# Kernel tuning notes

Hardware: AMD Instinct MI355X
Metric: run time of the kernel (lower is better)

The kernel has to match this reference:

```python
import jax, jax.numpy as jnp
import numpy as np

E, H, I, R, T, TOPK = 8, 1024, 2816, 8, 4096, 2
SCALING = 2.0  # lora_alpha / r = 16 / 8


def setup_inputs() -> dict:
    key = jax.random.key(0)
    ks = jax.random.split(key, 12)
    inp = {
        "hidden_states": jax.random.normal(ks[0], (T, H), dtype=jnp.float32),
        "routing_weights": jax.random.uniform(ks[1], (T, TOPK), dtype=jnp.float32),
        "selected_experts": jax.random.randint(ks[2], (T, TOPK), 0, E),
        # frozen base expert weights, (G, K, N) layout
        "gate_proj": jax.random.normal(ks[3], (E, H, I), dtype=jnp.float32) * 0.02,
        "up_proj": jax.random.normal(ks[4], (E, H, I), dtype=jnp.float32) * 0.02,
        "down_proj": jax.random.normal(ks[5], (E, I, H), dtype=jnp.float32) * 0.02,
        # LoRA adapters, A: [E, in, r], B: [E, r, out]  (B random, not zero, so delta is exercised)
        "gate_A": jax.random.normal(ks[6], (E, H, R), dtype=jnp.float32) * 0.02,
        "gate_B": jax.random.normal(ks[7], (E, R, I), dtype=jnp.float32) * 0.02,
        "up_A": jax.random.normal(ks[8], (E, H, R), dtype=jnp.float32) * 0.02,
        "up_B": jax.random.normal(ks[9], (E, R, I), dtype=jnp.float32) * 0.02,
        "down_A": jax.random.normal(ks[10], (E, I, R), dtype=jnp.float32) * 0.02,
        "down_B": jax.random.normal(ks[11], (E, R, H), dtype=jnp.float32) * 0.02,
    }
    return inp


def _moe_lora_forward(x, routing_weights, selected_experts,
                      gate_proj, up_proj, down_proj,
                      gate_A, gate_B, up_A, up_B, down_A, down_B):
    # combine weights per (token, expert): [T, E]
    combine = jnp.sum(
        jax.nn.one_hot(selected_experts, E, dtype=x.dtype) * routing_weights[..., None],
        axis=1,
    )
    out = jnp.zeros_like(x)
    for e in range(E):  # static small loop over experts
        g = x @ gate_proj[e] + SCALING * ((x @ gate_A[e]) @ gate_B[e])
        u = x @ up_proj[e] + SCALING * ((x @ up_A[e]) @ up_B[e])
        h = jax.nn.silu(g) * u  # [T, I]
        y = h @ down_proj[e] + SCALING * ((h @ down_A[e]) @ down_B[e])  # [T, H]
        out = out + combine[:, e:e + 1] * y
    return out


def reference(hidden_states, routing_weights, selected_experts,
              gate_proj, up_proj, down_proj,
              gate_A, gate_B, up_A, up_B, down_A, down_B):
    return _moe_lora_forward(hidden_states, routing_weights, selected_experts,
                             gate_proj, up_proj, down_proj,
                             gate_A, gate_B, up_A, up_B, down_A, down_B)
```

## Files before the change

### kernel.cpp

```cpp
#include <hip/hip_runtime.h>
#include <stdint.h>

#define T_TOK 4096
#define NE 8
#define HH 1024
#define II 2816
#define HE 1056
#define IEW 2944
#define HT 23
#define RRK 8
#define NPAIR (T_TOK*2)
#define ROWCAP 10240
#define MT_MAX 40
#define SCAL 2.0f

typedef short v8s __attribute__((ext_vector_type(8)));
typedef float v4f __attribute__((ext_vector_type(4)));

__device__ __forceinline__ unsigned short f2bf(float f){
  union { float f; unsigned u; } c; c.f = f;
  unsigned u = c.u;
  u += 0x7FFFu + ((u >> 16) & 1u);
  return (unsigned short)(u >> 16);
}
__device__ __forceinline__ float bf2f(unsigned short h){
  union { unsigned u; float f; } c; c.u = ((unsigned)h) << 16;
  return c.f;
}
__device__ __forceinline__ void gload16(const void* g, void* l){
  __builtin_amdgcn_global_load_lds(
      (const __attribute__((address_space(1))) unsigned int*)g,
      (__attribute__((address_space(3))) unsigned int*)l, 16, 0, 0);
}
__device__ __forceinline__ void fence_(){ asm volatile("" ::: "memory"); }

__global__ void route_count(const int* __restrict__ sel, int* __restrict__ counts,
                            int* __restrict__ bases, int* __restrict__ tile_e,
                            int* __restrict__ tile_r0){
  __shared__ int c[NE];
  int tid = threadIdx.x;
  if (tid < NE) c[tid] = 0;
  __syncthreads();
  for (int p = tid; p < NPAIR; p += 256) atomicAdd(&c[sel[p]], 1);
  __syncthreads();
  if (tid == 0){
    int b = 0;
    for (int e = 0; e < NE; e++){ counts[e] = c[e]; bases[e] = b; b += ((c[e] + 255) >> 8) << 8; }
    bases[NE] = b;
    int t = 0;
    for (int e = 0; e < NE; e++){
      int nt = (c[e] + 255) >> 8;
      for (int i = 0; i < nt; i++){ tile_e[t] = e; tile_r0[t] = bases[e] + i * 256; t++; }
    }
    for (; t < MT_MAX; t++){ tile_e[t] = -1; tile_r0[t] = 0; }
  }
}

__global__ void route_fill(const int* __restrict__ sel, const float* __restrict__ rw,
                           const int* __restrict__ bases,
                           int* __restrict__ row_token, int* __restrict__ row_expert,
                           float* __restrict__ row_w, int* __restrict__ pair2row){
  int e = blockIdx.x;
  int lane = threadIdx.x;
  if (e == NE){
    for (int idx = bases[NE] + lane; idx < ROWCAP; idx += 64){
      row_token[idx] = -1; row_expert[idx] = 0; row_w[idx] = 0.f;
    }
    return;
  }
  int base = bases[e];
  int cnt = 0;
  for (int chunk = 0; chunk < NPAIR; chunk += 64){
    int p = chunk + lane;
    bool m = (sel[p] == e);
    unsigned long long mask = __ballot(m);
    if (m){
      int pos = __popcll(mask & ((1ull << lane) - 1ull));
      int dst = base + cnt + pos;
      row_token[dst] = p >> 1;
      row_expert[dst] = e;
      row_w[dst] = rw[p];
      pair2row[p] = dst;
    }
    cnt += __popcll(mask);
  }
  int nb = bases[e + 1];
  for (int idx = base + cnt + lane; idx < nb; idx += 64){
    row_token[idx] = -1; row_expert[idx] = e; row_w[idx] = 0.f;
  }
}

__global__ void transpose_cvt(const float* __restrict__ W, unsigned short* __restrict__ Wt,
                              int K, int N, int KE){
  int e = blockIdx.y;
  int tilesK = K >> 6;
  int kt = (blockIdx.x % tilesK) * 64;
  int nt = (blockIdx.x / tilesK) * 64;
  __shared__ float tile[64][65];
  int tid = threadIdx.x;
  int r = tid >> 2;
  int c0 = (tid & 3) * 16;
  const float* src = W + (size_t)e * K * N + (size_t)(kt + r) * N + nt + c0;
  #pragma unroll
  for (int i = 0; i < 4; i++){
    float4 v = *(const float4*)(src + i * 4);
    tile[r][c0 + i*4 + 0] = v.x; tile[r][c0 + i*4 + 1] = v.y;
    tile[r][c0 + i*4 + 2] = v.z; tile[r][c0 + i*4 + 3] = v.w;
  }
  __syncthreads();
  union { unsigned short us[16]; uint4 q[2]; } pk;
  #pragma unroll
  for (int j = 0; j < 16; j++) pk.us[j] = f2bf(tile[c0 + j][r]);
  unsigned short* dst = Wt + (size_t)e * N * KE + (size_t)(nt + r) * KE + kt + c0;
  *(uint4*)(dst) = pk.q[0];
  *(uint4*)(dst + 8) = pk.q[1];
}

__global__ void ext_fill_pair(unsigned short* __restrict__ Wtg, unsigned short* __restrict__ Wtu,
                              const float* __restrict__ gB, const float* __restrict__ uB){
  int idx = blockIdx.x * 256 + threadIdx.x;
  if (idx >= NE * II) return;
  int e = idx / II, n = idx % II;
  unsigned short* g = Wtg + ((size_t)e * II + n) * HE + HH;
  unsigned short* u = Wtu + ((size_t)e * II + n) * HE + HH;
  #pragma unroll
  for (int j = 0; j < 8; j++){
    g[j] = f2bf(gB[((size_t)e * RRK + j) * II + n]);
    u[j] = 0;
    g[8 + j] = 0;
    u[8 + j] = f2bf(uB[((size_t)e * RRK + j) * II + n]);
  }
  #pragma unroll
  for (int j = 16; j < 32; j++){ g[j] = 0; u[j] = 0; }
}

__global__ void ext_fill_down(unsigned short* __restrict__ Wtd, const float* __restrict__ dB){
  int idx = blockIdx.x * 256 + threadIdx.x;
  if (idx >= NE * HH) return;
  int e = idx / HH, n = idx % HH;
  unsigned short* d = Wtd + ((size_t)e * HH + n) * IEW + II;
  #pragma unroll
  for (int j = 0; j < 8; j++) d[j] = f2bf(dB[((size_t)e * RRK + j) * HH + n]);
  for (int j = 8; j < 128; j++) d[j] = 0;
}

__global__ void gather_x(const float* __restrict__ x, const int* __restrict__ row_token,
                         unsigned short* __restrict__ Xg){
  int p = blockIdx.x; int tid = threadIdx.x;
  int tok = row_token[p];
  float4 v = make_float4(0.f, 0.f, 0.f, 0.f);
  if (tok >= 0) v = *(const float4*)(x + (size_t)tok * HH + tid * 4);
  uint2 o;
  o.x = (unsigned)f2bf(v.x) | ((unsigned)f2bf(v.y) << 16);
  o.y = (unsigned)f2bf(v.z) | ((unsigned)f2bf(v.w) << 16);
  *(uint2*)(Xg + (size_t)p * HE + tid * 4) = o;
}

__global__ void xa_kernel(const float* __restrict__ x, const float* __restrict__ gA,
                          const float* __restrict__ uA, const int* __restrict__ row_token,
                          const int* __restrict__ row_expert,
                          unsigned short* __restrict__ Xg){
  int p = blockIdx.x; int tid = threadIdx.x;
  int tok = row_token[p]; int e = row_expert[p];
  float ag[8], au[8];
  #pragma unroll
  for (int r = 0; r < 8; r++){ ag[r] = 0.f; au[r] = 0.f; }
  if (tok >= 0){
    int k0 = tid * 4;
    float4 xv = *(const float4*)(x + (size_t)tok * HH + k0);
    const float* pg = gA + ((size_t)e * HH + k0) * RRK;
    const float* pu = uA + ((size_t)e * HH + k0) * RRK;
    float xs[4] = {xv.x, xv.y, xv.z, xv.w};
    #pragma unroll
    for (int j = 0; j < 4; j++){
      #pragma unroll
      for (int r = 0; r < 8; r++){
        ag[r] += xs[j] * pg[j * RRK + r];
        au[r] += xs[j] * pu[j * RRK + r];
      }
    }
  }
  __shared__ float redg[8][4], redu[8][4];
  int lane = tid & 63, wv = tid >> 6;
  #pragma unroll
  for (int r = 0; r < 8; r++){
    float v1 = ag[r], v2 = au[r];
    for (int off = 32; off > 0; off >>= 1){ v1 += __shfl_down(v1, off); v2 += __shfl_down(v2, off); }
    if (lane == 0){ redg[r][wv] = v1; redu[r][wv] = v2; }
  }
  __syncthreads();
  if (tid < 8)
    Xg[(size_t)p * HE + HH + tid] = f2bf(SCAL * (redg[tid][0] + redg[tid][1] + redg[tid][2] + redg[tid][3]));
  else if (tid < 16){
    int r = tid - 8;
    Xg[(size_t)p * HE + HH + 8 + r] = f2bf(SCAL * (redu[r][0] + redu[r][1] + redu[r][2] + redu[r][3]));
  } else if (tid < 32){
    Xg[(size_t)p * HE + HH + tid] = 0;
  }
}

__global__ void ha_kernel(const unsigned short* __restrict__ hbuf, const float* __restrict__ dA,
                          const int* __restrict__ row_expert, unsigned short* __restrict__ hout){
  int p = blockIdx.x; int tid = threadIdx.x;
  int e = row_expert[p];
  float a[8];
  #pragma unroll
  for (int r = 0; r < 8; r++) a[r] = 0.f;
  for (int i = 0; i < 11; i++){
    int k = i * 256 + tid;
    float hv = bf2f(hbuf[(size_t)(k >> 7) * (ROWCAP * 128) + (size_t)p * 128 + (k & 127)]);
    const float* pd = dA + ((size_t)e * II + k) * RRK;
    #pragma unroll
    for (int r = 0; r < 8; r++) a[r] += hv * pd[r];
  }
  __shared__ float red[8][4];
  int lane = tid & 63, wv = tid >> 6;
  #pragma unroll
  for (int r = 0; r < 8; r++){
    float v = a[r];
    for (int off = 32; off > 0; off >>= 1) v += __shfl_down(v, off);
    if (lane == 0) red[r][wv] = v;
  }
  __syncthreads();
  unsigned short* ext = hout + (size_t)22 * (ROWCAP * 128) + (size_t)p * 128;
  if (tid < 8)
    ext[tid] = f2bf(SCAL * (red[tid][0] + red[tid][1] + red[tid][2] + red[tid][3]));
  else if (tid < 128)
    ext[tid] = 0;
}

__launch_bounds__(512, 2)
__global__ void gemm1_kernel(const unsigned short* __restrict__ Xg,
                             const unsigned short* __restrict__ Wtg,
                             const unsigned short* __restrict__ Wtu,
                             const int* __restrict__ tile_e,
                             const int* __restrict__ tile_r0,
                             unsigned short* __restrict__ hbuf){
  int hw = blockIdx.x;
  int lg = (hw & 7) * 110 + (hw >> 3);
  int mt = lg / 22;
  int n0 = (lg % 22) * 128;

  int e = tile_e[mt];
  if (e < 0) return;
  int row0 = tile_r0[mt];

  __shared__ unsigned short lds[2][4 * 4096];
  int tid = threadIdx.x;
  int lane = tid & 63;
  int w = tid >> 6;
  int wm = w >> 1;
  int wn = w & 1;
  int g = lane >> 4, r16 = lane & 15;

  const unsigned short* srcA = Xg + (size_t)row0 * HE;
  const unsigned short* srcG = Wtg + ((size_t)e * II + n0) * HE;
  const unsigned short* srcU = Wtu + ((size_t)e * II + n0) * HE;

  v4f accg[4][4], accu[4][4];
  #pragma unroll
  for (int i = 0; i < 4; i++)
    #pragma unroll
    for (int j = 0; j < 4; j++){
      accg[i][j] = (v4f){0.f, 0.f, 0.f, 0.f};
      accu[i][j] = (v4f){0.f, 0.f, 0.f, 0.f};
    }

  int uA0 = tid, uA1 = tid + 512;
  int rA0 = uA0 >> 2, rA1 = uA1 >> 2;
  size_t gA0 = (size_t)rA0 * HE + ((uA0 & 3) ^ ((rA0 >> 1) & 3)) * 8;
  size_t gA1 = (size_t)rA1 * HE + ((uA1 & 3) ^ ((rA1 >> 1) & 3)) * 8;
  int lA0 = (uA0 & ~63) * 8, lA1 = (uA1 & ~63) * 8;
  int rB = tid >> 2;
  size_t gB = (size_t)rB * HE + ((tid & 3) ^ ((rB >> 1) & 3)) * 8;
  int lB = (tid & ~63) * 8;

  const int NT = HE / 32;

  {
    unsigned short* buf = lds[0];
    gload16(srcA + gA0, buf + lA0);
    gload16(srcA + gA1, buf + lA1);
    gload16(srcG + gB, buf + 8192 + lB);
    gload16(srcU + gB, buf + 12288 + lB);
  }

  for (int t = 0; t < NT; t++){
    if (t + 1 < NT){
      unsigned short* nbuf = lds[(t + 1) & 1];
      int ks = (t + 1) * 32;
      gload16(srcA + gA0 + ks, nbuf + lA0);
      gload16(srcA + gA1 + ks, nbuf + lA1);
      gload16(srcG + gB + ks, nbuf + 8192 + lB);
      gload16(srcU + gB + ks, nbuf + 12288 + lB);
      asm volatile("s_waitcnt vmcnt(4)" ::: "memory");
    } else {
      asm volatile("s_waitcnt vmcnt(0)" ::: "memory");
    }
    __builtin_amdgcn_s_barrier();
    fence_();
    const unsigned short* buf = lds[t & 1];
    v8s a[4], bg[4], bu[4];
    #pragma unroll
    for (int f = 0; f < 4; f++){
      int rowA = wm * 64 + f * 16 + r16;
      int ca = g ^ ((rowA >> 1) & 3);
      a[f] = *(const v8s*)(buf + rowA * 32 + ca * 8);
      int rowB = wn * 64 + f * 16 + r16;
      int cb = g ^ ((rowB >> 1) & 3);
      bg[f] = *(const v8s*)(buf + 8192 + rowB * 32 + cb * 8);
      bu[f] = *(const v8s*)(buf + 12288 + rowB * 32 + cb * 8);
    }
    #pragma unroll
    for (int fm = 0; fm < 4; fm++)
      #pragma unroll
      for (int fn = 0; fn < 4; fn++){
        accg[fm][fn] = __builtin_amdgcn_mfma_f32_16x16x32_bf16(a[fm], bg[fn], accg[fm][fn], 0, 0, 0);
        accu[fm][fn] = __builtin_amdgcn_mfma_f32_16x16x32_bf16(a[fm], bu[fn], accu[fm][fn], 0, 0, 0);
      }
    fence_();
    __builtin_amdgcn_s_barrier();
    fence_();
  }

  unsigned short* sh = (unsigned short*)lds;
  #pragma unroll
  for (int fm = 0; fm < 4; fm++)
    #pragma unroll
    for (int fn = 0; fn < 4; fn++)
      #pragma unroll
      for (int r = 0; r < 4; r++){
        int lrow = wm * 64 + fm * 16 + g * 4 + r;
        int lcol = wn * 64 + fn * 16 + r16;
        float gg = accg[fm][fn][r];
        float uu = accu[fm][fn][r];
        float hh = (gg / (1.f + __expf(-gg))) * uu;
        int ch = (lcol >> 3) ^ (lrow & 7);
        sh[lrow * 128 + ch * 8 + (lcol & 7)] = f2bf(hh);
      }
  __syncthreads();
  unsigned short* dst = hbuf + ((size_t)(n0 >> 7) * ROWCAP + row0) * 128;
  #pragma unroll
  for (int pass = 0; pass < 8; pass++){
    int idx2 = pass * 512 + tid;
    int row = idx2 >> 4;
    int ch = idx2 & 15;
    int chs = ch ^ (row & 7);
    v8s val = *(const v8s*)(sh + row * 128 + chs * 8);
    *(v8s*)(dst + row * 128 + ch * 8) = val;
  }
}

__launch_bounds__(512, 2)
__global__ void gemm2_kernel(const unsigned short* __restrict__ hbuf,
                             const unsigned short* __restrict__ Wtd,
                             const int* __restrict__ tile_e,
                             const int* __restrict__ tile_r0,
                             const float* __restrict__ row_w,
                             float* __restrict__ Y){
  int hw = blockIdx.x;
  int lg = (hw & 7) * 40 + (hw >> 3);
  int mt = lg / 8;
  int n0 = (lg % 8) * 128;

  int e = tile_e[mt];
  if (e < 0) return;
  int row0 = tile_r0[mt];

  __shared__ unsigned short lds[2][3 * 4096];
  int tid = threadIdx.x;
  int lane = tid & 63;
  int w = tid >> 6;
  int wm = w >> 1, wn = w & 1;
  int g = lane >> 4, r16 = lane & 15;

  const unsigned short* srcA = hbuf + (size_t)row0 * 128;
  const unsigned short* srcB = Wtd + ((size_t)e * HH + n0) * IEW;

  v4f acc[4][4];
  #pragma unroll
  for (int i = 0; i < 4; i++)
    #pragma unroll
    for (int j = 0; j < 4; j++) acc[i][j] = (v4f){0.f, 0.f, 0.f, 0.f};

  int uA0 = tid, uA1 = tid + 512;
  int rA0 = uA0 >> 2, rA1 = uA1 >> 2;
  int cA0 = (uA0 & 3) ^ ((rA0 >> 1) & 3), cA1 = (uA1 & 3) ^ ((rA1 >> 1) & 3);
  size_t aoff0 = (size_t)rA0 * 128 + cA0 * 8;
  size_t aoff1 = (size_t)rA1 * 128 + cA1 * 8;
  int lA0 = (uA0 & ~63) * 8, lA1 = (uA1 & ~63) * 8;
  int rB = tid >> 2;
  int cB = (tid & 3) ^ ((rB >> 1) & 3);
  size_t boff = (size_t)rB * IEW + cB * 8;
  int lB = (tid & ~63) * 8;

  const int NT = IEW / 32;

  {
    unsigned short* buf = lds[0];
    gload16(srcA + aoff0, buf + lA0);
    gload16(srcA + aoff1, buf + lA1);
    gload16(srcB + boff, buf + 8192 + lB);
  }

  for (int t = 0; t < NT; t++){
    if (t + 1 < NT){
      unsigned short* nbuf = lds[(t + 1) & 1];
      int ks = (t + 1) * 32;
      size_t abase = (size_t)(ks >> 7) * (ROWCAP * 128) + (ks & 127);
      gload16(srcA + abase + aoff0, nbuf + lA0);
      gload16(srcA + abase + aoff1, nbuf + lA1);
      gload16(srcB + (size_t)ks + boff, nbuf + 8192 + lB);
      asm volatile("s_waitcnt vmcnt(3)" ::: "memory");
    } else {
      asm volatile("s_waitcnt vmcnt(0)" ::: "memory");
    }
    __builtin_amdgcn_s_barrier();
    fence_();
    const unsigned short* buf = lds[t & 1];
    v8s a[4], b[4];
    #pragma unroll
    for (int f = 0; f < 4; f++){
      int rowA = wm * 64 + f * 16 + r16;
      int ca = g ^ ((rowA >> 1) & 3);
      a[f] = *(const v8s*)(buf + rowA * 32 + ca * 8);
      int rowB = wn * 64 + f * 16 + r16;
      int cb = g ^ ((rowB >> 1) & 3);
      b[f] = *(const v8s*)(buf + 8192 + rowB * 32 + cb * 8);
    }
    #pragma unroll
    for (int fm = 0; fm < 4; fm++)
      #pragma unroll
      for (int fn = 0; fn < 4; fn++)
        acc[fm][fn] = __builtin_amdgcn_mfma_f32_16x16x32_bf16(a[fm], b[fn], acc[fm][fn], 0, 0, 0);
    fence_();
    __builtin_amdgcn_s_barrier();
    fence_();
  }

  #pragma unroll
  for (int fm = 0; fm < 4; fm++){
    #pragma unroll
    for (int r = 0; r < 4; r++){
      int lrow = wm * 64 + fm * 16 + g * 4 + r;
      int grow = row0 + lrow;
      float wgt = row_w[grow];
      #pragma unroll
      for (int fn = 0; fn < 4; fn++){
        int lcol = wn * 64 + fn * 16 + r16;
        Y[(size_t)grow * HH + n0 + lcol] = wgt * acc[fm][fn][r];
      }
    }
  }
}

__global__ void combine_kernel(const float* __restrict__ Y, const int* __restrict__ pair2row,
                               float* __restrict__ out){
  int t = blockIdx.x;
  int c = threadIdx.x * 4;
  int r0 = pair2row[2 * t];
  int r1 = pair2row[2 * t + 1];
  float4 a = *(const float4*)(Y + (size_t)r0 * HH + c);
  float4 b = *(const float4*)(Y + (size_t)r1 * HH + c);
  float4 o = make_float4(a.x + b.x, a.y + b.y, a.z + b.z, a.w + b.w);
  *(float4*)(out + (size_t)t * HH + c) = o;
}

extern "C" void kernel_launch(void* const* d_in, const int* in_sizes, int n_in,
                              void* d_out, int out_size, void* d_ws, size_t ws_size,
                              hipStream_t stream){
  const float* x         = (const float*)d_in[0];
  const float* rw        = (const float*)d_in[1];
  const int*   sel       = (const int*)d_in[2];
  const float* gate_proj = (const float*)d_in[3];
  const float* up_proj   = (const float*)d_in[4];
  const float* down_proj = (const float*)d_in[5];
  const float* gate_A    = (const float*)d_in[6];
  const float* gate_B    = (const float*)d_in[7];
  const float* up_A      = (const float*)d_in[8];
  const float* up_B      = (const float*)d_in[9];
  const float* down_A    = (const float*)d_in[10];
  const float* down_B    = (const float*)d_in[11];
  float* out = (float*)d_out;
  char* ws = (char*)d_ws;

  constexpr size_t OFF_COUNTS = 0;
  constexpr size_t OFF_BASES  = 256;
  constexpr size_t OFF_TILE_E = 512;
  constexpr size_t OFF_TILE_R0 = 1024;
  constexpr size_t OFF_ROWTOK = 2048;
  constexpr size_t OFF_ROWEXP = OFF_ROWTOK + (size_t)ROWCAP * 4;
  constexpr size_t OFF_ROWW   = OFF_ROWEXP + (size_t)ROWCAP * 4;
  constexpr size_t OFF_P2R    = OFF_ROWW + (size_t)ROWCAP * 4;
  constexpr size_t OFF_XG     = OFF_P2R + (size_t)NPAIR * 4;
  constexpr size_t OFF_H      = OFF_XG + (size_t)ROWCAP * HE * 2;
  constexpr size_t OFF_WTG    = OFF_H + (size_t)HT * ROWCAP * 128 * 2;
  constexpr size_t OFF_WTU    = OFF_WTG + (size_t)NE * II * HE * 2;
  constexpr size_t OFF_WTD    = OFF_WTU + (size_t)NE * II * HE * 2;
  constexpr size_t OFF_Y      = OFF_WTG;

  int* counts    = (int*)(ws + OFF_COUNTS);
  int* bases     = (int*)(ws + OFF_BASES);
  int* tile_e    = (int*)(ws + OFF_TILE_E);
  int* tile_r0   = (int*)(ws + OFF_TILE_R0);
  int* row_token = (int*)(ws + OFF_ROWTOK);
  int* row_expert= (int*)(ws + OFF_ROWEXP);
  float* row_w   = (float*)(ws + OFF_ROWW);
  int* pair2row  = (int*)(ws + OFF_P2R);
  unsigned short* Xg   = (unsigned short*)(ws + OFF_XG);
  unsigned short* hbuf = (unsigned short*)(ws + OFF_H);
  unsigned short* Wtg  = (unsigned short*)(ws + OFF_WTG);
  unsigned short* Wtu  = (unsigned short*)(ws + OFF_WTU);
  unsigned short* Wtd  = (unsigned short*)(ws + OFF_WTD);
  float* Y = (float*)(ws + OFF_Y);

  route_count<<<1, 256, 0, stream>>>(sel, counts, bases, tile_e, tile_r0);
  route_fill<<<NE + 1, 64, 0, stream>>>(sel, rw, bases, row_token, row_expert, row_w, pair2row);
  transpose_cvt<<<dim3((HH >> 6) * (II >> 6), NE), 256, 0, stream>>>(gate_proj, Wtg, HH, II, HE);
  transpose_cvt<<<dim3((HH >> 6) * (II >> 6), NE), 256, 0, stream>>>(up_proj, Wtu, HH, II, HE);
  transpose_cvt<<<dim3((II >> 6) * (HH >> 6), NE), 256, 0, stream>>>(down_proj, Wtd, II, HH, IEW);
  ext_fill_pair<<<(NE * II + 255) / 256, 256, 0, stream>>>(Wtg, Wtu, gate_B, up_B);
  ext_fill_down<<<(NE * HH + 255) / 256, 256, 0, stream>>>(Wtd, down_B);
  gather_x<<<ROWCAP, 256, 0, stream>>>(x, row_token, Xg);
  xa_kernel<<<ROWCAP, 256, 0, stream>>>(x, gate_A, up_A, row_token, row_expert, Xg);
  gemm1_kernel<<<MT_MAX * (II / 128), 512, 0, stream>>>(Xg, Wtg, Wtu, tile_e, tile_r0, hbuf);
  ha_kernel<<<ROWCAP, 256, 0, stream>>>(hbuf, down_A, row_expert, hbuf);
  gemm2_kernel<<<MT_MAX * (HH / 128), 512, 0, stream>>>(hbuf, Wtd, tile_e, tile_r0, row_w, Y);
  combine_kernel<<<T_TOK, 256, 0, stream>>>(Y, pair2row, out);
}
```

Before: 559.1 us.

## Widen down-proj GEMM tile to 128x256 and fuse x gather with LoRA-A projection

```diff
diff --git a/kernel.cpp b/kernel.cpp
--- a/kernel.cpp
+++ b/kernel.cpp
@@ -144,30 +144,24 @@
   for (int j = 8; j < 128; j++) d[j] = 0;
 }
 
-__global__ void gather_x(const float* __restrict__ x, const int* __restrict__ row_token,
-                         unsigned short* __restrict__ Xg){
-  int p = blockIdx.x; int tid = threadIdx.x;
-  int tok = row_token[p];
-  float4 v = make_float4(0.f, 0.f, 0.f, 0.f);
-  if (tok >= 0) v = *(const float4*)(x + (size_t)tok * HH + tid * 4);
-  uint2 o;
-  o.x = (unsigned)f2bf(v.x) | ((unsigned)f2bf(v.y) << 16);
-  o.y = (unsigned)f2bf(v.z) | ((unsigned)f2bf(v.w) << 16);
-  *(uint2*)(Xg + (size_t)p * HE + tid * 4) = o;
-}
-
-__global__ void xa_kernel(const float* __restrict__ x, const float* __restrict__ gA,
-                          const float* __restrict__ uA, const int* __restrict__ row_token,
-                          const int* __restrict__ row_expert,
-                          unsigned short* __restrict__ Xg){
+__global__ void gxa_kernel(const float* __restrict__ x, const float* __restrict__ gA,
+                           const float* __restrict__ uA, const int* __restrict__ row_token,
+                           const int* __restrict__ row_expert,
+                           unsigned short* __restrict__ Xg){
   int p = blockIdx.x; int tid = threadIdx.x;
   int tok = row_token[p]; int e = row_expert[p];
+  int k0 = tid * 4;
+  float4 xv = make_float4(0.f, 0.f, 0.f, 0.f);
+  if (tok >= 0) xv = *(const float4*)(x + (size_t)tok * HH + k0);
+  uint2 o;
+  o.x = (unsigned)f2bf(xv.x) | ((unsigned)f2bf(xv.y) << 16);
+  o.y = (unsigned)f2bf(xv.z) | ((unsigned)f2bf(xv.w) << 16);
+  *(uint2*)(Xg + (size_t)p * HE + k0) = o;
+
   float ag[8], au[8];
   #pragma unroll
   for (int r = 0; r < 8; r++){ ag[r] = 0.f; au[r] = 0.f; }
   if (tok >= 0){
-    int k0 = tid * 4;
-    float4 xv = *(const float4*)(x + (size_t)tok * HH + k0);
     const float* pg = gA + ((size_t)e * HH + k0) * RRK;
     const float* pu = uA + ((size_t)e * HH + k0) * RRK;
     float xs[4] = {xv.x, xv.y, xv.z, xv.w};
@@ -359,48 +353,48 @@
                              const float* __restrict__ row_w,
                              float* __restrict__ Y){
   int hw = blockIdx.x;
-  int lg = (hw & 7) * 40 + (hw >> 3);
-  int mt = lg / 8;
-  int n0 = (lg % 8) * 128;
+  int lg = (hw & 7) * 20 + (hw >> 3);
+  int mt = lg / 4;
+  int n0 = (lg % 4) * 256;
 
   int e = tile_e[mt];
   if (e < 0) return;
   int row0 = tile_r0[mt];
 
-  __shared__ unsigned short lds[2][3 * 4096];
+  __shared__ unsigned short lds[2][2 * 8192];
   int tid = threadIdx.x;
   int lane = tid & 63;
   int w = tid >> 6;
-  int wm = w >> 1, wn = w & 1;
+  int wm = w >> 1;
+  int wn = w & 1;
   int g = lane >> 4, r16 = lane & 15;
 
   const unsigned short* srcA = hbuf + (size_t)row0 * 128;
   const unsigned short* srcB = Wtd + ((size_t)e * HH + n0) * IEW;
 
-  v4f acc[4][4];
+  v4f acc[4][8];
   #pragma unroll
   for (int i = 0; i < 4; i++)
     #pragma unroll
-    for (int j = 0; j < 4; j++) acc[i][j] = (v4f){0.f, 0.f, 0.f, 0.f};
-
-  int uA0 = tid, uA1 = tid + 512;
-  int rA0 = uA0 >> 2, rA1 = uA1 >> 2;
-  int cA0 = (uA0 & 3) ^ ((rA0 >> 1) & 3), cA1 = (uA1 & 3) ^ ((rA1 >> 1) & 3);
-  size_t aoff0 = (size_t)rA0 * 128 + cA0 * 8;
-  size_t aoff1 = (size_t)rA1 * 128 + cA1 * 8;
-  int lA0 = (uA0 & ~63) * 8, lA1 = (uA1 & ~63) * 8;
-  int rB = tid >> 2;
-  int cB = (tid & 3) ^ ((rB >> 1) & 3);
-  size_t boff = (size_t)rB * IEW + cB * 8;
-  int lB = (tid & ~63) * 8;
+    for (int j = 0; j < 8; j++) acc[i][j] = (v4f){0.f, 0.f, 0.f, 0.f};
+
+  int u0 = tid, u1 = tid + 512;
+  int r0_ = u0 >> 2, r1_ = u1 >> 2;
+  int c0_ = (u0 & 3) ^ ((r0_ >> 1) & 3), c1_ = (u1 & 3) ^ ((r1_ >> 1) & 3);
+  size_t aoff0 = (size_t)r0_ * 128 + c0_ * 8;
+  size_t aoff1 = (size_t)r1_ * 128 + c1_ * 8;
+  size_t boff0 = (size_t)r0_ * IEW + c0_ * 8;
+  size_t boff1 = (size_t)r1_ * IEW + c1_ * 8;
+  int l0 = (u0 & ~63) * 8, l1 = (u1 & ~63) * 8;
 
   const int NT = IEW / 32;
 
   {
     unsigned short* buf = lds[0];
-    gload16(srcA + aoff0, buf + lA0);
-    gload16(srcA + aoff1, buf + lA1);
-    gload16(srcB + boff, buf + 8192 + lB);
+    gload16(srcA + aoff0, buf + l0);
+    gload16(srcA + aoff1, buf + l1);
+    gload16(srcB + boff0, buf + 8192 + l0);
+    gload16(srcB + boff1, buf + 8192 + l1);
   }
 
   for (int t = 0; t < NT; t++){
@@ -408,30 +402,34 @@
       unsigned short* nbuf = lds[(t + 1) & 1];
       int ks = (t + 1) * 32;
       size_t abase = (size_t)(ks >> 7) * (ROWCAP * 128) + (ks & 127);
-      gload16(srcA + abase + aoff0, nbuf + lA0);
-      gload16(srcA + abase + aoff1, nbuf + lA1);
-      gload16(srcB + (size_t)ks + boff, nbuf + 8192 + lB);
-      asm volatile("s_waitcnt vmcnt(3)" ::: "memory");
+      gload16(srcA + abase + aoff0, nbuf + l0);
+      gload16(srcA + abase + aoff1, nbuf + l1);
+      gload16(srcB + (size_t)ks + boff0, nbuf + 8192 + l0);
+      gload16(srcB + (size_t)ks + boff1, nbuf + 8192 + l1);
+      asm volatile("s_waitcnt vmcnt(4)" ::: "memory");
     } else {
       asm volatile("s_waitcnt vmcnt(0)" ::: "memory");
     }
     __builtin_amdgcn_s_barrier();
     fence_();
     const unsigned short* buf = lds[t & 1];
-    v8s a[4], b[4];
+    v8s a[4], b[8];
     #pragma unroll
     for (int f = 0; f < 4; f++){
       int rowA = wm * 64 + f * 16 + r16;
       int ca = g ^ ((rowA >> 1) & 3);
       a[f] = *(const v8s*)(buf + rowA * 32 + ca * 8);
-      int rowB = wn * 64 + f * 16 + r16;
+    }
+    #pragma unroll
+    for (int fn = 0; fn < 8; fn++){
+      int rowB = wn * 128 + fn * 16 + r16;
       int cb = g ^ ((rowB >> 1) & 3);
-      b[f] = *(const v8s*)(buf + 8192 + rowB * 32 + cb * 8);
+      b[fn] = *(const v8s*)(buf + 8192 + rowB * 32 + cb * 8);
     }
     #pragma unroll
     for (int fm = 0; fm < 4; fm++)
       #pragma unroll
-      for (int fn = 0; fn < 4; fn++)
+      for (int fn = 0; fn < 8; fn++)
         acc[fm][fn] = __builtin_amdgcn_mfma_f32_16x16x32_bf16(a[fm], b[fn], acc[fm][fn], 0, 0, 0);
     fence_();
     __builtin_amdgcn_s_barrier();
@@ -446,8 +444,8 @@
       int grow = row0 + lrow;
       float wgt = row_w[grow];
       #pragma unroll
-      for (int fn = 0; fn < 4; fn++){
-        int lcol = wn * 64 + fn * 16 + r16;
+      for (int fn = 0; fn < 8; fn++){
+        int lcol = wn * 128 + fn * 16 + r16;
         Y[(size_t)grow * HH + n0 + lcol] = wgt * acc[fm][fn][r];
       }
     }
@@ -521,10 +519,9 @@
   transpose_cvt<<<dim3((II >> 6) * (HH >> 6), NE), 256, 0, stream>>>(down_proj, Wtd, II, HH, IEW);
   ext_fill_pair<<<(NE * II + 255) / 256, 256, 0, stream>>>(Wtg, Wtu, gate_B, up_B);
   ext_fill_down<<<(NE * HH + 255) / 256, 256, 0, stream>>>(Wtd, down_B);
-  gather_x<<<ROWCAP, 256, 0, stream>>>(x, row_token, Xg);
-  xa_kernel<<<ROWCAP, 256, 0, stream>>>(x, gate_A, up_A, row_token, row_expert, Xg);
+  gxa_kernel<<<ROWCAP, 256, 0, stream>>>(x, gate_A, up_A, row_token, row_expert, Xg);
   gemm1_kernel<<<MT_MAX * (II / 128), 512, 0, stream>>>(Xg, Wtg, Wtu, tile_e, tile_r0, hbuf);
   ha_kernel<<<ROWCAP, 256, 0, stream>>>(hbuf, down_A, row_expert, hbuf);
-  gemm2_kernel<<<MT_MAX * (HH / 128), 512, 0, stream>>>(hbuf, Wtd, tile_e, tile_r0, row_w, Y);
+  gemm2_kernel<<<MT_MAX * (HH / 256), 512, 0, stream>>>(hbuf, Wtd, tile_e, tile_r0, row_w, Y);
   combine_kernel<<<T_TOK, 256, 0, stream>>>(Y, pair2row, out);
 }
```

New measurement: 556.3 us. Within noise of the previous version (-0.5%).
